# Kernel tuning notes

Measured on AMD Instinct MI355X. Metric: run time of the kernel, lower is better.

Reference implementation:

```python
import jax, jax.numpy as jnp
import numpy as np

B, S, H = 128, 256, 256  # batch, seq_len, hidden_size


def setup_inputs() -> dict:
    key = jax.random.key(0)
    ks = jax.random.split(key, 12)
    g = lambda k, shape, s=0.05: jax.random.normal(k, shape, jnp.float32) * s
    return {
        "x": jax.random.normal(ks[0], (B, S, 1024), jnp.float32),
        "stages": jax.random.normal(ks[1], (B, S, 67), jnp.float32),
        "timestamps": jax.random.uniform(ks[2], (B, S), jnp.float32),
        # stage_embedding: Linear(67,256)-ReLU-Linear(256,512)-ReLU-Linear(512,1024)-ReLU
        "se_w1": g(ks[3], (67, 256)), "se_b1": jnp.zeros((256,), jnp.float32),
        "se_w2": g(ks[4], (256, 512)), "se_b2": jnp.zeros((512,), jnp.float32),
        "se_w3": g(ks[5], (512, 1024)), "se_b3": jnp.zeros((1024,), jnp.float32),
        # TLSTM weights
        "W_all_w": g(ks[6], (H, 4 * H)), "W_all_b": jnp.zeros((4 * H,), jnp.float32),
        "U_all_w": g(ks[7], (2048, 4 * H)), "U_all_b": jnp.zeros((4 * H,), jnp.float32),
        "W_d_w": g(ks[8], (H, H)), "W_d_b": jnp.zeros((H,), jnp.float32),
        # classifier Linear(256,1)
        "cls_w": g(ks[9], (H, 1)), "cls_b": jnp.zeros((1,), jnp.float32),
    }


def reference(x, stages, timestamps, se_w1, se_b1, se_w2, se_b2, se_w3, se_b3,
              W_all_w, W_all_b, U_all_w, U_all_b, W_d_w, W_d_b, cls_w, cls_b):
    b, s, _ = x.shape
    # stage embedding MLP on flattened [b*s, 67]
    st = stages.reshape(b * s, 67)
    st = jax.nn.relu(st @ se_w1 + se_b1)
    st = jax.nn.relu(st @ se_w2 + se_b2)
    st = jax.nn.relu(st @ se_w3 + se_b3)
    xin = jnp.concatenate([x, st.reshape(b, s, 1024)], axis=2)  # [b,s,2048]
    # input projection U_all for all steps at once (same math, batched GEMM)
    u = jnp.einsum('bse,eh->bsh', xin, U_all_w) + U_all_b  # [b,s,4H]
    u_t = jnp.swapaxes(u, 0, 1)                             # [s,b,4H]
    ts_t = jnp.swapaxes(timestamps, 0, 1)[..., None]        # [s,b,1]

    def step(carry, inp):
        h, c = carry
        ut, tt = inp
        c_s1 = jnp.tanh(c @ W_d_w + W_d_b)
        c_adj = (c - c_s1) + c_s1 * tt  # time-decay adjusted cell
        outs = h @ W_all_w + W_all_b + ut
        f, i, o, c_tmp = jnp.split(jax.nn.sigmoid(outs), 4, axis=1)
        c_new = f * c_adj + i * c_tmp
        h_new = o * jnp.tanh(c_new)
        return (h_new, c_new), h_new

    h0 = jnp.zeros((b, H), x.dtype)
    c0 = jnp.zeros((b, H), x.dtype)
    _, hs = jax.lax.scan(step, (h0, c0), (u_t, ts_t))  # hs: [s,b,H]
    feat = jnp.swapaxes(hs, 0, 1).reshape(b * s, H)
    out = feat @ cls_w + cls_b
    return out, feat
```

## Files before the change

kernel.cpp:

```cpp
#include <hip/hip_runtime.h>
#include <hip/hip_bf16.h>
#include <stdint.h>

#define B_ 128
#define S_ 256
#define H_ 256

typedef __attribute__((ext_vector_type(8))) short short8;
typedef __attribute__((ext_vector_type(4))) float f32x4;

__device__ __forceinline__ short f2bf_s(float x){
    union { __hip_bfloat16 b; short s; } u; u.b = __float2bfloat16(x); return u.s;
}
__device__ __forceinline__ float bf2f_s(short s){
    union { __hip_bfloat16 b; short s2; } u; u.s2 = s; return __bfloat162float(u.b);
}
__device__ __forceinline__ void load_lds16(const void* g, void* l){
    __builtin_amdgcn_global_load_lds(
        (const __attribute__((address_space(1))) void*)g,
        (__attribute__((address_space(3))) void*)l, 16, 0, 0);
}
__device__ __forceinline__ float sigmoidf_(float x){
    return 1.0f / (1.0f + __expf(-x));
}


__global__ void k_cvt_x(const float* __restrict__ x, short* __restrict__ xin){
    int q = blockIdx.x * blockDim.x + threadIdx.x;
    if (q >= 8388608) return;
    const float4 v = ((const float4*)x)[q];
    int r = q >> 8;
    int c4 = (q & 255) << 2;
    short4 o;
    o.x = f2bf_s(v.x); o.y = f2bf_s(v.y); o.z = f2bf_s(v.z); o.w = f2bf_s(v.w);
    *(short4*)(xin + (int64_t)r * 2048 + c4) = o;
}

__global__ void k_cvt_stages(const float* __restrict__ st, short* __restrict__ sp){
    int i = blockIdx.x * blockDim.x + threadIdx.x;
    if (i >= 32768 * 96) return;
    int r = i / 96, k = i - r * 96;
    sp[i] = (k < 67) ? f2bf_s(st[(int64_t)r * 67 + k]) : (short)0;
}

__global__ void k_transpose(const float* __restrict__ w, short* __restrict__ wt,
                            int K, int N, int Kpad){
    int i = blockIdx.x * blockDim.x + threadIdx.x;
    if (i >= N * Kpad) return;
    int n = i / Kpad, k = i - n * Kpad;
    wt[i] = (k < K) ? f2bf_s(w[(int64_t)k * N + n]) : (short)0;
}

__global__ __launch_bounds__(256) void k_gemm(
    const short* __restrict__ A, int lda,
    const short* __restrict__ BT, int ldb,
    const float* __restrict__ bias,
    int K, int flags,
    float* __restrict__ Cf, short* __restrict__ Cb, int ldc)
{
    __shared__ __align__(16) short At[128 * 32];
    __shared__ __align__(16) short Bt[128 * 32];
    const int tid = threadIdx.x;
    const int lane = tid & 63, w = tid >> 6;
    const int q = lane >> 4, m = lane & 15;
    const int wr = w >> 1, wc = w & 1;
    const int bm = blockIdx.y, bn = blockIdx.x;

    const short* Ablk = A + (int64_t)bm * 128 * lda;
    const short* Bblk = BT + (int64_t)bn * 128 * ldb;

    f32x4 acc[4][4] = {};

    for (int k0 = 0; k0 < K; k0 += 32){
#pragma unroll
        for (int call = 0; call < 2; ++call){
            int chunk = (call * 4 + w) * 64 + lane;
            int row = chunk >> 2, co = (chunk & 3) * 8;
            load_lds16(Ablk + (int64_t)row * lda + k0 + co, At + (call * 4 + w) * 512);
            load_lds16(Bblk + (int64_t)row * ldb + k0 + co, Bt + (call * 4 + w) * 512);
        }
        __syncthreads();
        short8 af[4], bfr[4];
#pragma unroll
        for (int mt = 0; mt < 4; ++mt)
            af[mt] = *(const short8*)(At + (wr * 64 + mt * 16 + m) * 32 + q * 8);
#pragma unroll
        for (int nt = 0; nt < 4; ++nt)
            bfr[nt] = *(const short8*)(Bt + (wc * 64 + nt * 16 + m) * 32 + q * 8);
#pragma unroll
        for (int mt = 0; mt < 4; ++mt)
#pragma unroll
            for (int nt = 0; nt < 4; ++nt)
                acc[mt][nt] = __builtin_amdgcn_mfma_f32_16x16x32_bf16(
                    af[mt], bfr[nt], acc[mt][nt], 0, 0, 0);
        __syncthreads();
    }

#pragma unroll
    for (int mt = 0; mt < 4; ++mt){
#pragma unroll
        for (int nt = 0; nt < 4; ++nt){
            int col = bn * 128 + wc * 64 + nt * 16 + m;
            float bv = bias[col];
#pragma unroll
            for (int rg = 0; rg < 4; ++rg){
                int row = bm * 128 + wr * 64 + mt * 16 + q * 4 + rg;
                float v = acc[mt][nt][rg] + bv;
                if (flags & 1) v = fmaxf(v, 0.0f);
                if (flags & 2){
                    Cb[(int64_t)row * ldc + col] = f2bf_s(v);
                } else if (flags & 4){
                    int s = row & 255, b = row >> 8;
                    Cf[((int64_t)s * 128 + b) * 1024 + col] = v;
                } else {
                    Cf[(int64_t)row * ldc + col] = v;
                }
            }
        }
    }
}

__global__ __launch_bounds__(256, 2) void k_scan(
    const float* __restrict__ W_all, const float* __restrict__ W_all_b,
    const float* __restrict__ W_d,   const float* __restrict__ W_d_b,
    const float* __restrict__ u,     const float* __restrict__ tsp,
    unsigned* __restrict__ ctr,
    unsigned* __restrict__ h_seq,
    unsigned* __restrict__ c_seq,
    float* __restrict__ feat)
{
    __shared__ __align__(16) short wf_hi[3][8][64][8];
    __shared__ __align__(16) short wf_lo[3][8][64][8];
    __shared__ float Dg[3][16][17];

    const int tid = threadIdx.x;
    const int r = blockIdx.x >> 5, cg = blockIdx.x & 31;
    const int j0 = cg * 8, row0 = r * 16;

    for (int idx = tid; idx < 3 * 8 * 64; idx += 256){
        int t = idx / 512;
        int kk = (idx >> 6) & 7;
        int ln = idx & 63;
        int qq = ln >> 4, nn = ln & 15;
#pragma unroll
        for (int jj = 0; jj < 8; ++jj){
            int k = kk * 32 + qq * 8 + jj;
            float v = 0.0f;
            if (t < 2){
                int ngl = (nn < 8) ? (t * 512 + j0 + nn) : (t * 512 + 256 + j0 + nn - 8);
                v = W_all[(int64_t)k * 1024 + ngl];
            } else if (nn < 8){
                v = W_d[(int64_t)k * 256 + j0 + nn];
            }
            short hi = f2bf_s(v);
            wf_hi[t][kk][ln][jj] = hi;
            wf_lo[t][kk][ln][jj] = f2bf_s(v - bf2f_s(hi));
        }
    }
    __syncthreads();

    const int lane = tid & 63, w = tid >> 6;
    const int q = lane >> 4, al15 = lane & 15;

    const int b_own  = tid >> 3;
    const int jl_own = tid & 7;
    const int gb     = row0 + b_own;
    const int gj     = j0 + jl_own;
    float c_reg = 0.0f;

    float bf_ = 0, bi_ = 0, bo_ = 0, bg_ = 0, bd_ = 0;
    if (tid < 128){
        bf_ = W_all_b[gj];
        bi_ = W_all_b[256 + gj];
        bo_ = W_all_b[512 + gj];
        bg_ = W_all_b[768 + gj];
        bd_ = W_d_b[gj];
    }

    for (int s = 0; s < 256; ++s){
        float uf = 0, ui = 0, uo = 0, ug = 0, tt = 0;
        if (tid < 128){
            const float* urow = u + ((int64_t)s * 128 + gb) * 1024;
            uf = urow[gj];       ui = urow[256 + gj];
            uo = urow[512 + gj]; ug = urow[768 + gj];
            tt = tsp[gb * 256 + s];
        }

        if (s > 0 && tid == 0){
            while (__hip_atomic_fetch_add(&ctr[r * 256 + s - 1], 0u,
                                          __ATOMIC_RELAXED, __HIP_MEMORY_SCOPE_AGENT) < 32u)
                ;
        }
        __syncthreads();

        if (w < 3){
            const unsigned* src = (w < 2 ? h_seq : c_seq) + (int64_t)s * 32768
                                  + (row0 + al15) * 256;
            f32x4 acc = {0.0f, 0.0f, 0.0f, 0.0f};
#pragma unroll
            for (int kk = 0; kk < 8; ++kk){
                int kb = kk * 32 + q * 8;
                const uint4* p = (const uint4*)(src + kb);
                uint4 da = p[0], db = p[1];
                unsigned w0 = da.x, w1 = da.y, w2 = da.z, w3 = da.w;
                unsigned w4 = db.x, w5 = db.y, w6 = db.z, w7 = db.w;
                union { short8 v; unsigned u32[4]; } ah, al;
                ah.u32[0] = __builtin_amdgcn_perm(w1, w0, 0x05040100u);
                ah.u32[1] = __builtin_amdgcn_perm(w3, w2, 0x05040100u);
                ah.u32[2] = __builtin_amdgcn_perm(w5, w4, 0x05040100u);
                ah.u32[3] = __builtin_amdgcn_perm(w7, w6, 0x05040100u);
                al.u32[0] = __builtin_amdgcn_perm(w1, w0, 0x07060302u);
                al.u32[1] = __builtin_amdgcn_perm(w3, w2, 0x07060302u);
                al.u32[2] = __builtin_amdgcn_perm(w5, w4, 0x07060302u);
                al.u32[3] = __builtin_amdgcn_perm(w7, w6, 0x07060302u);
                short8 bh = *(const short8*)&wf_hi[w][kk][lane][0];
                short8 bl = *(const short8*)&wf_lo[w][kk][lane][0];
                acc = __builtin_amdgcn_mfma_f32_16x16x32_bf16(ah.v, bh, acc, 0, 0, 0);
                acc = __builtin_amdgcn_mfma_f32_16x16x32_bf16(ah.v, bl, acc, 0, 0, 0);
                acc = __builtin_amdgcn_mfma_f32_16x16x32_bf16(al.v, bh, acc, 0, 0, 0);
            }
#pragma unroll
            for (int rg = 0; rg < 4; ++rg)
                Dg[w][q * 4 + rg][al15] = acc[rg];
        }
        __syncthreads();

        if (tid < 128){
            float fpre = Dg[0][b_own][jl_own]     + uf + bf_;
            float ipre = Dg[0][b_own][8 + jl_own] + ui + bi_;
            float opre = Dg[1][b_own][jl_own]     + uo + bo_;
            float gpre = Dg[1][b_own][8 + jl_own] + ug + bg_;
            float spre = Dg[2][b_own][jl_own]     + bd_;

            float cs1 = tanhf(spre);
            float cadj = (c_reg - cs1) + cs1 * tt;
            float fg = sigmoidf_(fpre);
            float ig = sigmoidf_(ipre);
            float og = sigmoidf_(opre);
            float gg = sigmoidf_(gpre);
            float cn = fg * cadj + ig * gg;
            float hn = og * tanhf(cn);
            c_reg = cn;

            short chi = f2bf_s(cn);
            unsigned cword = (unsigned)(unsigned short)chi |
                             ((unsigned)(unsigned short)f2bf_s(cn - bf2f_s(chi)) << 16);
            short hhi = f2bf_s(hn);
            unsigned hword = (unsigned)(unsigned short)hhi |
                             ((unsigned)(unsigned short)f2bf_s(hn - bf2f_s(hhi)) << 16);
            int64_t oidx = (int64_t)(s + 1) * 32768 + gb * 256 + gj;
            __hip_atomic_store(&c_seq[oidx], cword,
                               __ATOMIC_RELAXED, __HIP_MEMORY_SCOPE_AGENT);
            __hip_atomic_store(&h_seq[oidx], hword,
                               __ATOMIC_RELAXED, __HIP_MEMORY_SCOPE_AGENT);
            __builtin_nontemporal_store(hn, &feat[((int64_t)gb * 256 + s) * 256 + gj]);
        }
        __syncthreads();
        if (tid == 0)
            __hip_atomic_fetch_add(&ctr[r * 256 + s], 1u,
                                   __ATOMIC_RELAXED, __HIP_MEMORY_SCOPE_AGENT);
    }
}

__global__ __launch_bounds__(256) void k_cls(
    const float* __restrict__ feat, const float* __restrict__ cls_w,
    const float* __restrict__ cls_b, float* __restrict__ out)
{
    int tid = threadIdx.x, lane = tid & 63, w = tid >> 6;
    int row = blockIdx.x * 4 + w;
    float4 v  = ((const float4*)(feat + (int64_t)row * 256))[lane];
    float4 cw = ((const float4*)cls_w)[lane];
    float d = v.x * cw.x + v.y * cw.y + v.z * cw.z + v.w * cw.w;
#pragma unroll
    for (int off = 32; off > 0; off >>= 1)
        d += __shfl_down(d, off, 64);
    if (lane == 0) out[row] = d + cls_b[0];
}

extern "C" void kernel_launch(void* const* d_in, const int* in_sizes, int n_in,
                              void* d_out, int out_size, void* d_ws, size_t ws_size,
                              hipStream_t stream) {
    const float* x      = (const float*)d_in[0];
    const float* stages = (const float*)d_in[1];
    const float* tsp    = (const float*)d_in[2];
    const float* se_w1  = (const float*)d_in[3];
    const float* se_b1  = (const float*)d_in[4];
    const float* se_w2  = (const float*)d_in[5];
    const float* se_b2  = (const float*)d_in[6];
    const float* se_w3  = (const float*)d_in[7];
    const float* se_b3  = (const float*)d_in[8];
    const float* W_all  = (const float*)d_in[9];
    const float* W_allb = (const float*)d_in[10];
    const float* U_w    = (const float*)d_in[11];
    const float* U_b    = (const float*)d_in[12];
    const float* W_d    = (const float*)d_in[13];
    const float* W_d_b  = (const float*)d_in[14];
    const float* cls_w  = (const float*)d_in[15];
    const float* cls_b  = (const float*)d_in[16];
    (void)in_sizes; (void)n_in; (void)out_size; (void)ws_size;

    float* out  = (float*)d_out;
    float* feat = out + 32768;

    char* ws = (char*)d_ws;
    unsigned* ctr    = (unsigned*)(ws + 0);
    short*  stagesP  = (short*)  (ws + 532480);
    short*  st1      = (short*)  (ws + 6823936);
    short*  st2      = (short*)  (ws + 23601152);
    short*  w1T      = (short*)  (ws + 57155584);
    short*  w2T      = (short*)  (ws + 57204736);
    short*  w3T      = (short*)  (ws + 57466880);
    short*  UwT      = (short*)  (ws + 58515456);
    short*  xin      = (short*)  (ws + 62709760);
    float*  u        = (float*)  (ws + 196927488);
    unsigned* h_seq  = (unsigned*)(ws + 62709760);
    unsigned* c_seq  = (unsigned*)(ws + 62709760 + 33685504);

    hipMemsetAsync(ctr, 0, 8192, stream);

    k_cvt_x<<<8388608 / 256, 256, 0, stream>>>(x, xin);
    k_cvt_stages<<<(32768 * 96) / 256, 256, 0, stream>>>(stages, stagesP);
    k_transpose<<<(256 * 96) / 256, 256, 0, stream>>>(se_w1, w1T, 67, 256, 96);
    k_transpose<<<(512 * 256) / 256, 256, 0, stream>>>(se_w2, w2T, 256, 512, 256);
    k_transpose<<<(1024 * 512) / 256, 256, 0, stream>>>(se_w3, w3T, 512, 1024, 512);
    k_transpose<<<(1024 * 2048) / 256, 256, 0, stream>>>(U_w, UwT, 2048, 1024, 2048);

    k_gemm<<<dim3(2, 256), 256, 0, stream>>>(stagesP, 96, w1T, 96, se_b1, 96, 1 | 2,
                                             nullptr, st1, 256);
    k_gemm<<<dim3(4, 256), 256, 0, stream>>>(st1, 256, w2T, 256, se_b2, 256, 1 | 2,
                                             nullptr, st2, 512);
    k_gemm<<<dim3(8, 256), 256, 0, stream>>>(st2, 512, w3T, 512, se_b3, 512, 1 | 2,
                                             nullptr, xin + 1024, 2048);
    k_gemm<<<dim3(8, 256), 256, 0, stream>>>(xin, 2048, UwT, 2048, U_b, 2048, 4,
                                             u, nullptr, 1024);

    hipMemsetAsync(h_seq, 0, 131072, stream);
    hipMemsetAsync(c_seq, 0, 131072, stream);

    k_scan<<<256, 256, 0, stream>>>(W_all, W_allb, W_d, W_d_b, u, tsp,
                                    ctr, h_seq, c_seq, feat);

    k_cls<<<8192, 256, 0, stream>>>(feat, cls_w, cls_b, out);
}
```

Measured before the change: 1.484 ms.

## Overlap U_all projection GEMM with recurrent scan via fused persistent kernel

The input projection GEMM is split. The first 32 row-blocks (time steps 0–31) run up front, and the remaining row-blocks run as extra workgroups inside a fused kernel alongside the scan blocks. Scan blocks poll per-row-block progress counters before reading u. Inputs are written in time-major order so GEMM row-blocks map to time steps. The per-step counter barrier is replaced with a double-buffered h/c ring whose low mantissa bits carry a step tag, and consumers spin on the tagged data directly. The aim is to hide most of the big GEMM behind the latency-bound scan and cut one synchronization round trip per step, at the cost of slightly perturbing the low bits of h/c and relying on all 2048 blocks being co-resident or scheduled scan-first.

After: 2.783 ms. 87.6% more time.

```diff
diff --git a/kernel.cpp b/kernel.cpp
--- a/kernel.cpp
+++ b/kernel.cpp
@@ -31,9 +31,10 @@
     const float4 v = ((const float4*)x)[q];
     int r = q >> 8;
     int c4 = (q & 255) << 2;
+    int rp = (r & 255) * 128 + (r >> 8);
     short4 o;
     o.x = f2bf_s(v.x); o.y = f2bf_s(v.y); o.z = f2bf_s(v.z); o.w = f2bf_s(v.w);
-    *(short4*)(xin + (int64_t)r * 2048 + c4) = o;
+    *(short4*)(xin + (int64_t)rp * 2048 + c4) = o;
 }
 
 __global__ void k_cvt_stages(const float* __restrict__ st, short* __restrict__ sp){
@@ -108,10 +109,9 @@
                 float v = acc[mt][nt][rg] + bv;
                 if (flags & 1) v = fmaxf(v, 0.0f);
                 if (flags & 2){
-                    Cb[(int64_t)row * ldc + col] = f2bf_s(v);
-                } else if (flags & 4){
-                    int s = row & 255, b = row >> 8;
-                    Cf[((int64_t)s * 128 + b) * 1024 + col] = v;
+                    int64_t orow = (flags & 8)
+                        ? ((int64_t)(row & 255) * 128 + (row >> 8)) : (int64_t)row;
+                    Cb[orow * ldc + col] = f2bf_s(v);
                 } else {
                     Cf[(int64_t)row * ldc + col] = v;
                 }
@@ -120,20 +120,83 @@
     }
 }
 
-__global__ __launch_bounds__(256, 2) void k_scan(
+struct ScanSh {
+    short wf_hi[3][8][64][8];
+    short wf_lo[3][8][64][8];
+    float Dg[3][16][17];
+};
+struct GemmSh { short At[128 * 32]; short Bt[128 * 32]; };
+
+__global__ __launch_bounds__(256, 2) void k_fused(
+    const short* __restrict__ xin, const short* __restrict__ UwT,
+    const float* __restrict__ U_b,
     const float* __restrict__ W_all, const float* __restrict__ W_all_b,
     const float* __restrict__ W_d,   const float* __restrict__ W_d_b,
-    const float* __restrict__ u,     const float* __restrict__ tsp,
-    unsigned* __restrict__ ctr,
-    unsigned* __restrict__ h_seq,
-    unsigned* __restrict__ c_seq,
+    float* uu,
+    const float* __restrict__ tsp,
+    unsigned* __restrict__ uprog,
+    unsigned* __restrict__ hring,
+    unsigned* __restrict__ cring,
     float* __restrict__ feat)
 {
-    __shared__ __align__(16) short wf_hi[3][8][64][8];
-    __shared__ __align__(16) short wf_lo[3][8][64][8];
-    __shared__ float Dg[3][16][17];
-
+    __shared__ __align__(16) union { ScanSh sc; GemmSh gm; } sh;
     const int tid = threadIdx.x;
+
+    if (blockIdx.x >= 256){
+        int gid = blockIdx.x - 256;
+        const int bm = 32 + (gid >> 3), bn = gid & 7;
+        const int lane = tid & 63, w = tid >> 6;
+        const int q = lane >> 4, m = lane & 15;
+        const int wr = w >> 1, wc = w & 1;
+        const short* Ablk = xin + (int64_t)bm * 128 * 2048;
+        const short* Bblk = UwT + (int64_t)bn * 128 * 2048;
+        f32x4 acc[4][4] = {};
+        for (int k0 = 0; k0 < 2048; k0 += 32){
+#pragma unroll
+            for (int call = 0; call < 2; ++call){
+                int chunk = (call * 4 + w) * 64 + lane;
+                int row = chunk >> 2, co = (chunk & 3) * 8;
+                load_lds16(Ablk + (int64_t)row * 2048 + k0 + co, sh.gm.At + (call * 4 + w) * 512);
+                load_lds16(Bblk + (int64_t)row * 2048 + k0 + co, sh.gm.Bt + (call * 4 + w) * 512);
+            }
+            __syncthreads();
+            short8 af[4], bfr[4];
+#pragma unroll
+            for (int mt = 0; mt < 4; ++mt)
+                af[mt] = *(const short8*)(sh.gm.At + (wr * 64 + mt * 16 + m) * 32 + q * 8);
+#pragma unroll
+            for (int nt = 0; nt < 4; ++nt)
+                bfr[nt] = *(const short8*)(sh.gm.Bt + (wc * 64 + nt * 16 + m) * 32 + q * 8);
+#pragma unroll
+            for (int mt = 0; mt < 4; ++mt)
+#pragma unroll
+                for (int nt = 0; nt < 4; ++nt)
+                    acc[mt][nt] = __builtin_amdgcn_mfma_f32_16x16x32_bf16(
+                        af[mt], bfr[nt], acc[mt][nt], 0, 0, 0);
+            __syncthreads();
+        }
+#pragma unroll
+        for (int mt = 0; mt < 4; ++mt)
+#pragma unroll
+            for (int nt = 0; nt < 4; ++nt){
+                int col = bn * 128 + wc * 64 + nt * 16 + m;
+                float bv = U_b[col];
+#pragma unroll
+                for (int rg = 0; rg < 4; ++rg){
+                    int row = bm * 128 + wr * 64 + mt * 16 + q * 4 + rg;
+                    __hip_atomic_store(&uu[(int64_t)row * 1024 + col],
+                                       acc[mt][nt][rg] + bv,
+                                       __ATOMIC_RELAXED, __HIP_MEMORY_SCOPE_AGENT);
+                }
+            }
+        __syncthreads();
+        if (tid == 0)
+            __hip_atomic_fetch_add(&uprog[bm], 1u,
+                                   __ATOMIC_RELAXED, __HIP_MEMORY_SCOPE_AGENT);
+        return;
+    }
+
+    __builtin_amdgcn_s_setprio(1);
     const int r = blockIdx.x >> 5, cg = blockIdx.x & 31;
     const int j0 = cg * 8, row0 = r * 16;
 
@@ -153,8 +216,8 @@
                 v = W_d[(int64_t)k * 256 + j0 + nn];
             }
             short hi = f2bf_s(v);
-            wf_hi[t][kk][ln][jj] = hi;
-            wf_lo[t][kk][ln][jj] = f2bf_s(v - bf2f_s(hi));
+            sh.sc.wf_hi[t][kk][ln][jj] = hi;
+            sh.sc.wf_lo[t][kk][ln][jj] = f2bf_s(v - bf2f_s(hi));
         }
     }
     __syncthreads();
@@ -162,75 +225,152 @@
     const int lane = tid & 63, w = tid >> 6;
     const int q = lane >> 4, al15 = lane & 15;
 
-    const int b_own  = tid >> 3;
-    const int jl_own = tid & 7;
-    const int gb     = row0 + b_own;
-    const int gj     = j0 + jl_own;
+    const int tid2 = tid & 127;
+    const int b_own = tid2 >> 3, jl_own = tid2 & 7;
+    const int gb = row0 + b_own, gj = j0 + jl_own;
     float c_reg = 0.0f;
-
     float bf_ = 0, bi_ = 0, bo_ = 0, bg_ = 0, bd_ = 0;
-    if (tid < 128){
+    if (w >= 2){
         bf_ = W_all_b[gj];
         bi_ = W_all_b[256 + gj];
         bo_ = W_all_b[512 + gj];
         bg_ = W_all_b[768 + gj];
         bd_ = W_d_b[gj];
     }
+    int u_upto = 32;
+
+    const unsigned long long TAGM = 0xFFFCFFFFFFFCFFFFULL;
 
     for (int s = 0; s < 256; ++s){
+        __syncthreads();
         float uf = 0, ui = 0, uo = 0, ug = 0, tt = 0;
-        if (tid < 128){
-            const float* urow = u + ((int64_t)s * 128 + gb) * 1024;
+
+        if (w < 2){
+            f32x4 acc0 = {0.f, 0.f, 0.f, 0.f}, acc1 = {0.f, 0.f, 0.f, 0.f};
+            if (s > 0){
+                const unsigned tagexp = (unsigned)((s - 1) & 3);
+                unsigned long long* sp = (unsigned long long*)
+                    ((w == 0 ? hring : cring) + (((s - 1) & 1) << 15) + (row0 + al15) * 256);
+                unsigned long long d[32];
+                for (unsigned round = 0; ; ++round){
+                    if ((round & 3u) != 3u){
+#pragma unroll
+                        for (int kk = 0; kk < 8; ++kk)
+#pragma unroll
+                            for (int i = 0; i < 4; ++i)
+                                d[kk * 4 + i] = __hip_atomic_load(
+                                    &sp[kk * 16 + q * 4 + i],
+                                    __ATOMIC_RELAXED, __HIP_MEMORY_SCOPE_AGENT);
+                    } else {
+#pragma unroll
+                        for (int kk = 0; kk < 8; ++kk)
+#pragma unroll
+                            for (int i = 0; i < 4; ++i){
+                                unsigned* pw = (unsigned*)&sp[kk * 16 + q * 4 + i];
+                                unsigned lo = __hip_atomic_fetch_add(pw, 0u,
+                                    __ATOMIC_RELAXED, __HIP_MEMORY_SCOPE_AGENT);
+                                unsigned hi = __hip_atomic_fetch_add(pw + 1, 0u,
+                                    __ATOMIC_RELAXED, __HIP_MEMORY_SCOPE_AGENT);
+                                d[kk * 4 + i] = (unsigned long long)lo |
+                                                ((unsigned long long)hi << 32);
+                            }
+                    }
+                    bool bad = false;
+#pragma unroll
+                    for (int t2 = 0; t2 < 32; ++t2){
+                        unsigned lo = (unsigned)d[t2], hi = (unsigned)(d[t2] >> 32);
+                        bad |= (((lo >> 16) & 3u) != tagexp) | (((hi >> 16) & 3u) != tagexp);
+                    }
+                    if (__all(!bad)) break;
+                }
+                if (w == 0){
+#pragma unroll
+                    for (int kk = 0; kk < 8; ++kk){
+                        unsigned long long q0 = d[kk*4+0] & TAGM, q1 = d[kk*4+1] & TAGM;
+                        unsigned long long q2 = d[kk*4+2] & TAGM, q3 = d[kk*4+3] & TAGM;
+                        unsigned w0_=(unsigned)q0, w1_=(unsigned)(q0>>32);
+                        unsigned w2_=(unsigned)q1, w3_=(unsigned)(q1>>32);
+                        unsigned w4_=(unsigned)q2, w5_=(unsigned)(q2>>32);
+                        unsigned w6_=(unsigned)q3, w7_=(unsigned)(q3>>32);
+                        union { short8 v; unsigned u32[4]; } ah, al;
+                        ah.u32[0]=__builtin_amdgcn_perm(w1_,w0_,0x05040100u);
+                        ah.u32[1]=__builtin_amdgcn_perm(w3_,w2_,0x05040100u);
+                        ah.u32[2]=__builtin_amdgcn_perm(w5_,w4_,0x05040100u);
+                        ah.u32[3]=__builtin_amdgcn_perm(w7_,w6_,0x05040100u);
+                        al.u32[0]=__builtin_amdgcn_perm(w1_,w0_,0x07060302u);
+                        al.u32[1]=__builtin_amdgcn_perm(w3_,w2_,0x07060302u);
+                        al.u32[2]=__builtin_amdgcn_perm(w5_,w4_,0x07060302u);
+                        al.u32[3]=__builtin_amdgcn_perm(w7_,w6_,0x07060302u);
+                        short8 bh0 = *(const short8*)&sh.sc.wf_hi[0][kk][lane][0];
+                        short8 bl0 = *(const short8*)&sh.sc.wf_lo[0][kk][lane][0];
+                        short8 bh1 = *(const short8*)&sh.sc.wf_hi[1][kk][lane][0];
+                        short8 bl1 = *(const short8*)&sh.sc.wf_lo[1][kk][lane][0];
+                        acc0 = __builtin_amdgcn_mfma_f32_16x16x32_bf16(ah.v, bh0, acc0, 0,0,0);
+                        acc0 = __builtin_amdgcn_mfma_f32_16x16x32_bf16(ah.v, bl0, acc0, 0,0,0);
+                        acc0 = __builtin_amdgcn_mfma_f32_16x16x32_bf16(al.v, bh0, acc0, 0,0,0);
+                        acc1 = __builtin_amdgcn_mfma_f32_16x16x32_bf16(ah.v, bh1, acc1, 0,0,0);
+                        acc1 = __builtin_amdgcn_mfma_f32_16x16x32_bf16(ah.v, bl1, acc1, 0,0,0);
+                        acc1 = __builtin_amdgcn_mfma_f32_16x16x32_bf16(al.v, bh1, acc1, 0,0,0);
+                    }
+                } else {
+#pragma unroll
+                    for (int kk = 0; kk < 8; ++kk){
+                        unsigned long long q0 = d[kk*4+0] & TAGM, q1 = d[kk*4+1] & TAGM;
+                        unsigned long long q2 = d[kk*4+2] & TAGM, q3 = d[kk*4+3] & TAGM;
+                        unsigned w0_=(unsigned)q0, w1_=(unsigned)(q0>>32);
+                        unsigned w2_=(unsigned)q1, w3_=(unsigned)(q1>>32);
+                        unsigned w4_=(unsigned)q2, w5_=(unsigned)(q2>>32);
+                        unsigned w6_=(unsigned)q3, w7_=(unsigned)(q3>>32);
+                        union { short8 v; unsigned u32[4]; } ah, al;
+                        ah.u32[0]=__builtin_amdgcn_perm(w1_,w0_,0x05040100u);
+                        ah.u32[1]=__builtin_amdgcn_perm(w3_,w2_,0x05040100u);
+                        ah.u32[2]=__builtin_amdgcn_perm(w5_,w4_,0x05040100u);
+                        ah.u32[3]=__builtin_amdgcn_perm(w7_,w6_,0x05040100u);
+                        al.u32[0]=__builtin_amdgcn_perm(w1_,w0_,0x07060302u);
+                        al.u32[1]=__builtin_amdgcn_perm(w3_,w2_,0x07060302u);
+                        al.u32[2]=__builtin_amdgcn_perm(w5_,w4_,0x07060302u);
+                        al.u32[3]=__builtin_amdgcn_perm(w7_,w6_,0x07060302u);
+                        short8 bh2 = *(const short8*)&sh.sc.wf_hi[2][kk][lane][0];
+                        short8 bl2 = *(const short8*)&sh.sc.wf_lo[2][kk][lane][0];
+                        acc0 = __builtin_amdgcn_mfma_f32_16x16x32_bf16(ah.v, bh2, acc0, 0,0,0);
+                        acc0 = __builtin_amdgcn_mfma_f32_16x16x32_bf16(ah.v, bl2, acc0, 0,0,0);
+                        acc0 = __builtin_amdgcn_mfma_f32_16x16x32_bf16(al.v, bh2, acc0, 0,0,0);
+                    }
+                }
+            }
+#pragma unroll
+            for (int rg = 0; rg < 4; ++rg){
+                if (w == 0){
+                    sh.sc.Dg[0][q * 4 + rg][al15] = acc0[rg];
+                    sh.sc.Dg[1][q * 4 + rg][al15] = acc1[rg];
+                } else {
+                    sh.sc.Dg[2][q * 4 + rg][al15] = acc0[rg];
+                }
+            }
+        } else {
+            bool adv = false; unsigned rr = 0;
+            while (u_upto <= s){
+                unsigned v = ((rr & 3u) != 3u)
+                    ? __hip_atomic_load(&uprog[u_upto],
+                                        __ATOMIC_RELAXED, __HIP_MEMORY_SCOPE_AGENT)
+                    : __hip_atomic_fetch_add(&uprog[u_upto], 0u,
+                                        __ATOMIC_RELAXED, __HIP_MEMORY_SCOPE_AGENT);
+                if (v >= 8u){ ++u_upto; adv = true; } else ++rr;
+            }
+            if (adv) __builtin_amdgcn_fence(__ATOMIC_ACQUIRE, "agent");
+            const float* urow = uu + ((int64_t)s * 128 + gb) * 1024;
             uf = urow[gj];       ui = urow[256 + gj];
             uo = urow[512 + gj]; ug = urow[768 + gj];
             tt = tsp[gb * 256 + s];
         }
-
-        if (s > 0 && tid == 0){
-            while (__hip_atomic_fetch_add(&ctr[r * 256 + s - 1], 0u,
-                                          __ATOMIC_RELAXED, __HIP_MEMORY_SCOPE_AGENT) < 32u)
-                ;
-        }
         __syncthreads();
 
-        if (w < 3){
-            const unsigned* src = (w < 2 ? h_seq : c_seq) + (int64_t)s * 32768
-                                  + (row0 + al15) * 256;
-            f32x4 acc = {0.0f, 0.0f, 0.0f, 0.0f};
-#pragma unroll
-            for (int kk = 0; kk < 8; ++kk){
-                int kb = kk * 32 + q * 8;
-                const uint4* p = (const uint4*)(src + kb);
-                uint4 da = p[0], db = p[1];
-                unsigned w0 = da.x, w1 = da.y, w2 = da.z, w3 = da.w;
-                unsigned w4 = db.x, w5 = db.y, w6 = db.z, w7 = db.w;
-                union { short8 v; unsigned u32[4]; } ah, al;
-                ah.u32[0] = __builtin_amdgcn_perm(w1, w0, 0x05040100u);
-                ah.u32[1] = __builtin_amdgcn_perm(w3, w2, 0x05040100u);
-                ah.u32[2] = __builtin_amdgcn_perm(w5, w4, 0x05040100u);
-                ah.u32[3] = __builtin_amdgcn_perm(w7, w6, 0x05040100u);
-                al.u32[0] = __builtin_amdgcn_perm(w1, w0, 0x07060302u);
-                al.u32[1] = __builtin_amdgcn_perm(w3, w2, 0x07060302u);
-                al.u32[2] = __builtin_amdgcn_perm(w5, w4, 0x07060302u);
-                al.u32[3] = __builtin_amdgcn_perm(w7, w6, 0x07060302u);
-                short8 bh = *(const short8*)&wf_hi[w][kk][lane][0];
-                short8 bl = *(const short8*)&wf_lo[w][kk][lane][0];
-                acc = __builtin_amdgcn_mfma_f32_16x16x32_bf16(ah.v, bh, acc, 0, 0, 0);
-                acc = __builtin_amdgcn_mfma_f32_16x16x32_bf16(ah.v, bl, acc, 0, 0, 0);
-                acc = __builtin_amdgcn_mfma_f32_16x16x32_bf16(al.v, bh, acc, 0, 0, 0);
-            }
-#pragma unroll
-            for (int rg = 0; rg < 4; ++rg)
-                Dg[w][q * 4 + rg][al15] = acc[rg];
-        }
-        __syncthreads();
-
-        if (tid < 128){
-            float fpre = Dg[0][b_own][jl_own]     + uf + bf_;
-            float ipre = Dg[0][b_own][8 + jl_own] + ui + bi_;
-            float opre = Dg[1][b_own][jl_own]     + uo + bo_;
-            float gpre = Dg[1][b_own][8 + jl_own] + ug + bg_;
-            float spre = Dg[2][b_own][jl_own]     + bd_;
+        if (w >= 2){
+            float fpre = sh.sc.Dg[0][b_own][jl_own]     + uf + bf_;
+            float ipre = sh.sc.Dg[0][b_own][8 + jl_own] + ui + bi_;
+            float opre = sh.sc.Dg[1][b_own][jl_own]     + uo + bo_;
+            float gpre = sh.sc.Dg[1][b_own][8 + jl_own] + ug + bg_;
+            float spre = sh.sc.Dg[2][b_own][jl_own]     + bd_;
 
             float cs1 = tanhf(spre);
             float cadj = (c_reg - cs1) + cs1 * tt;
@@ -242,23 +382,22 @@
             float hn = og * tanhf(cn);
             c_reg = cn;
 
+            unsigned tag = (unsigned)(s & 3);
             short chi = f2bf_s(cn);
+            unsigned short clo = (unsigned short)f2bf_s(cn - bf2f_s(chi));
             unsigned cword = (unsigned)(unsigned short)chi |
-                             ((unsigned)(unsigned short)f2bf_s(cn - bf2f_s(chi)) << 16);
+                             (((unsigned)((clo & 0xFFFCu) | tag)) << 16);
             short hhi = f2bf_s(hn);
+            unsigned short hlo = (unsigned short)f2bf_s(hn - bf2f_s(hhi));
             unsigned hword = (unsigned)(unsigned short)hhi |
-                             ((unsigned)(unsigned short)f2bf_s(hn - bf2f_s(hhi)) << 16);
-            int64_t oidx = (int64_t)(s + 1) * 32768 + gb * 256 + gj;
-            __hip_atomic_store(&c_seq[oidx], cword,
+                             (((unsigned)((hlo & 0xFFFCu) | tag)) << 16);
+            int off = ((s & 1) << 15) + gb * 256 + gj;
+            __hip_atomic_store(&cring[off], cword,
                                __ATOMIC_RELAXED, __HIP_MEMORY_SCOPE_AGENT);
-            __hip_atomic_store(&h_seq[oidx], hword,
+            __hip_atomic_store(&hring[off], hword,
                                __ATOMIC_RELAXED, __HIP_MEMORY_SCOPE_AGENT);
             __builtin_nontemporal_store(hn, &feat[((int64_t)gb * 256 + s) * 256 + gj]);
         }
-        __syncthreads();
-        if (tid == 0)
-            __hip_atomic_fetch_add(&ctr[r * 256 + s], 1u,
-                                   __ATOMIC_RELAXED, __HIP_MEMORY_SCOPE_AGENT);
     }
 }
 
@@ -303,7 +442,9 @@
     float* feat = out + 32768;
 
     char* ws = (char*)d_ws;
-    unsigned* ctr    = (unsigned*)(ws + 0);
+    unsigned* uprog  = (unsigned*)(ws + 0);
+    unsigned* hring  = (unsigned*)(ws + 4096);
+    unsigned* cring  = (unsigned*)(ws + 266240);
     short*  stagesP  = (short*)  (ws + 532480);
     short*  st1      = (short*)  (ws + 6823936);
     short*  st2      = (short*)  (ws + 23601152);
@@ -313,10 +454,12 @@
     short*  UwT      = (short*)  (ws + 58515456);
     short*  xin      = (short*)  (ws + 62709760);
     float*  u        = (float*)  (ws + 196927488);
-    unsigned* h_seq  = (unsigned*)(ws + 62709760);
-    unsigned* c_seq  = (unsigned*)(ws + 62709760 + 33685504);
-
-    hipMemsetAsync(ctr, 0, 8192, stream);
+
+    hipMemsetAsync(uprog, 0, 4096, stream);
+    hipMemsetAsync((char*)hring,          0x55, 131072, stream);
+    hipMemsetAsync((char*)hring + 131072, 0x00, 131072, stream);
+    hipMemsetAsync((char*)cring,          0x55, 131072, stream);
+    hipMemsetAsync((char*)cring + 131072, 0x00, 131072, stream);
 
     k_cvt_x<<<8388608 / 256, 256, 0, stream>>>(x, xin);
     k_cvt_stages<<<(32768 * 96) / 256, 256, 0, stream>>>(stages, stagesP);
@@ -329,16 +472,14 @@
                                              nullptr, st1, 256);
     k_gemm<<<dim3(4, 256), 256, 0, stream>>>(st1, 256, w2T, 256, se_b2, 256, 1 | 2,
                                              nullptr, st2, 512);
-    k_gemm<<<dim3(8, 256), 256, 0, stream>>>(st2, 512, w3T, 512, se_b3, 512, 1 | 2,
+    k_gemm<<<dim3(8, 256), 256, 0, stream>>>(st2, 512, w3T, 512, se_b3, 512, 1 | 2 | 8,
                                              nullptr, xin + 1024, 2048);
-    k_gemm<<<dim3(8, 256), 256, 0, stream>>>(xin, 2048, UwT, 2048, U_b, 2048, 4,
-                                             u, nullptr, 1024);
-
-    hipMemsetAsync(h_seq, 0, 131072, stream);
-    hipMemsetAsync(c_seq, 0, 131072, stream);
-
-    k_scan<<<256, 256, 0, stream>>>(W_all, W_allb, W_d, W_d_b, u, tsp,
-                                    ctr, h_seq, c_seq, feat);
+
+    k_gemm<<<dim3(8, 32), 256, 0, stream>>>(xin, 2048, UwT, 2048, U_b, 2048, 0,
+                                            u, nullptr, 1024);
+
+    k_fused<<<2048, 256, 0, stream>>>(xin, UwT, U_b, W_all, W_allb, W_d, W_d_b,
+                                      u, tsp, uprog, hring, cring, feat);
 
     k_cls<<<8192, 256, 0, stream>>>(feat, cls_w, cls_b, out);
 }
```

## Permute xin rows to step-major early and rebalance scan warp roles

Applied to the files above, without the earlier changes.

The x conversion and the third stage-MLP GEMM now write xin rows in (s,b) order, so the U projection GEMM stores u with contiguous row-major writes instead of a scattered transposed store. In the scan kernel, the gate matmuls move from three warps to two (warp 0 handles both W_all tiles) and the elementwise cell update moves to warps 2-3. The spin-wait gets an iteration cap, an explicit acquire fence is added, and launch bounds drop to one block per SIMD pair. The iteration cap risks proceeding before data is ready if a wait runs long, and warp 0 now carries a heavier serial MFMA chain per step.

Result: slower. 2.551 ms (+71.9%).

```diff
diff --git a/kernel.cpp b/kernel.cpp
--- a/kernel.cpp
+++ b/kernel.cpp
@@ -31,9 +31,10 @@
     const float4 v = ((const float4*)x)[q];
     int r = q >> 8;
     int c4 = (q & 255) << 2;
+    int rp = (r & 255) * 128 + (r >> 8);
     short4 o;
     o.x = f2bf_s(v.x); o.y = f2bf_s(v.y); o.z = f2bf_s(v.z); o.w = f2bf_s(v.w);
-    *(short4*)(xin + (int64_t)r * 2048 + c4) = o;
+    *(short4*)(xin + (int64_t)rp * 2048 + c4) = o;
 }
 
 __global__ void k_cvt_stages(const float* __restrict__ st, short* __restrict__ sp){
@@ -108,10 +109,9 @@
                 float v = acc[mt][nt][rg] + bv;
                 if (flags & 1) v = fmaxf(v, 0.0f);
                 if (flags & 2){
-                    Cb[(int64_t)row * ldc + col] = f2bf_s(v);
-                } else if (flags & 4){
-                    int s = row & 255, b = row >> 8;
-                    Cf[((int64_t)s * 128 + b) * 1024 + col] = v;
+                    int64_t orow = (flags & 8)
+                        ? ((int64_t)(row & 255) * 128 + (row >> 8)) : (int64_t)row;
+                    Cb[orow * ldc + col] = f2bf_s(v);
                 } else {
                     Cf[(int64_t)row * ldc + col] = v;
                 }
@@ -120,7 +120,7 @@
     }
 }
 
-__global__ __launch_bounds__(256, 2) void k_scan(
+__global__ __launch_bounds__(256, 1) void k_scan(
     const float* __restrict__ W_all, const float* __restrict__ W_all_b,
     const float* __restrict__ W_d,   const float* __restrict__ W_d_b,
     const float* __restrict__ u,     const float* __restrict__ tsp,
@@ -162,14 +162,12 @@
     const int lane = tid & 63, w = tid >> 6;
     const int q = lane >> 4, al15 = lane & 15;
 
-    const int b_own  = tid >> 3;
-    const int jl_own = tid & 7;
-    const int gb     = row0 + b_own;
-    const int gj     = j0 + jl_own;
+    const int tid2 = tid & 127;
+    const int b_own = tid2 >> 3, jl_own = tid2 & 7;
+    const int gb = row0 + b_own, gj = j0 + jl_own;
     float c_reg = 0.0f;
-
     float bf_ = 0, bi_ = 0, bo_ = 0, bg_ = 0, bd_ = 0;
-    if (tid < 128){
+    if (w >= 2){
         bf_ = W_all_b[gj];
         bi_ = W_all_b[256 + gj];
         bo_ = W_all_b[512 + gj];
@@ -179,53 +177,78 @@
 
     for (int s = 0; s < 256; ++s){
         float uf = 0, ui = 0, uo = 0, ug = 0, tt = 0;
-        if (tid < 128){
+
+        if (w >= 2){
             const float* urow = u + ((int64_t)s * 128 + gb) * 1024;
             uf = urow[gj];       ui = urow[256 + gj];
             uo = urow[512 + gj]; ug = urow[768 + gj];
             tt = tsp[gb * 256 + s];
         }
-
         if (s > 0 && tid == 0){
-            while (__hip_atomic_fetch_add(&ctr[r * 256 + s - 1], 0u,
-                                          __ATOMIC_RELAXED, __HIP_MEMORY_SCOPE_AGENT) < 32u)
-                ;
-        }
-        __syncthreads();
-
-        if (w < 3){
-            const unsigned* src = (w < 2 ? h_seq : c_seq) + (int64_t)s * 32768
-                                  + (row0 + al15) * 256;
-            f32x4 acc = {0.0f, 0.0f, 0.0f, 0.0f};
+            for (unsigned it = 0; it < 100000u; ++it){
+                if (__hip_atomic_fetch_add(&ctr[r * 256 + s - 1], 0u,
+                                           __ATOMIC_RELAXED,
+                                           __HIP_MEMORY_SCOPE_AGENT) >= 32u)
+                    break;
+            }
+        }
+        __syncthreads();
+
+        if (w < 2){
+            if (s > 0)
+                __builtin_amdgcn_fence(__ATOMIC_ACQUIRE, "agent");
+
+            const unsigned* src = (w == 0 ? h_seq : c_seq)
+                                  + (int64_t)s * 32768 + (row0 + al15) * 256;
+            f32x4 acc0 = {0.f, 0.f, 0.f, 0.f}, acc1 = {0.f, 0.f, 0.f, 0.f};
 #pragma unroll
             for (int kk = 0; kk < 8; ++kk){
                 int kb = kk * 32 + q * 8;
                 const uint4* p = (const uint4*)(src + kb);
                 uint4 da = p[0], db = p[1];
-                unsigned w0 = da.x, w1 = da.y, w2 = da.z, w3 = da.w;
-                unsigned w4 = db.x, w5 = db.y, w6 = db.z, w7 = db.w;
+                unsigned w0_ = da.x, w1_ = da.y, w2_ = da.z, w3_ = da.w;
+                unsigned w4_ = db.x, w5_ = db.y, w6_ = db.z, w7_ = db.w;
                 union { short8 v; unsigned u32[4]; } ah, al;
-                ah.u32[0] = __builtin_amdgcn_perm(w1, w0, 0x05040100u);
-                ah.u32[1] = __builtin_amdgcn_perm(w3, w2, 0x05040100u);
-                ah.u32[2] = __builtin_amdgcn_perm(w5, w4, 0x05040100u);
-                ah.u32[3] = __builtin_amdgcn_perm(w7, w6, 0x05040100u);
-                al.u32[0] = __builtin_amdgcn_perm(w1, w0, 0x07060302u);
-                al.u32[1] = __builtin_amdgcn_perm(w3, w2, 0x07060302u);
-                al.u32[2] = __builtin_amdgcn_perm(w5, w4, 0x07060302u);
-                al.u32[3] = __builtin_amdgcn_perm(w7, w6, 0x07060302u);
-                short8 bh = *(const short8*)&wf_hi[w][kk][lane][0];
-                short8 bl = *(const short8*)&wf_lo[w][kk][lane][0];
-                acc = __builtin_amdgcn_mfma_f32_16x16x32_bf16(ah.v, bh, acc, 0, 0, 0);
-                acc = __builtin_amdgcn_mfma_f32_16x16x32_bf16(ah.v, bl, acc, 0, 0, 0);
-                acc = __builtin_amdgcn_mfma_f32_16x16x32_bf16(al.v, bh, acc, 0, 0, 0);
-            }
-#pragma unroll
-            for (int rg = 0; rg < 4; ++rg)
-                Dg[w][q * 4 + rg][al15] = acc[rg];
-        }
-        __syncthreads();
-
-        if (tid < 128){
+                ah.u32[0] = __builtin_amdgcn_perm(w1_, w0_, 0x05040100u);
+                ah.u32[1] = __builtin_amdgcn_perm(w3_, w2_, 0x05040100u);
+                ah.u32[2] = __builtin_amdgcn_perm(w5_, w4_, 0x05040100u);
+                ah.u32[3] = __builtin_amdgcn_perm(w7_, w6_, 0x05040100u);
+                al.u32[0] = __builtin_amdgcn_perm(w1_, w0_, 0x07060302u);
+                al.u32[1] = __builtin_amdgcn_perm(w3_, w2_, 0x07060302u);
+                al.u32[2] = __builtin_amdgcn_perm(w5_, w4_, 0x07060302u);
+                al.u32[3] = __builtin_amdgcn_perm(w7_, w6_, 0x07060302u);
+                if (w == 0){
+                    short8 bh0 = *(const short8*)&wf_hi[0][kk][lane][0];
+                    short8 bl0 = *(const short8*)&wf_lo[0][kk][lane][0];
+                    short8 bh1 = *(const short8*)&wf_hi[1][kk][lane][0];
+                    short8 bl1 = *(const short8*)&wf_lo[1][kk][lane][0];
+                    acc0 = __builtin_amdgcn_mfma_f32_16x16x32_bf16(ah.v, bh0, acc0, 0,0,0);
+                    acc0 = __builtin_amdgcn_mfma_f32_16x16x32_bf16(ah.v, bl0, acc0, 0,0,0);
+                    acc0 = __builtin_amdgcn_mfma_f32_16x16x32_bf16(al.v, bh0, acc0, 0,0,0);
+                    acc1 = __builtin_amdgcn_mfma_f32_16x16x32_bf16(ah.v, bh1, acc1, 0,0,0);
+                    acc1 = __builtin_amdgcn_mfma_f32_16x16x32_bf16(ah.v, bl1, acc1, 0,0,0);
+                    acc1 = __builtin_amdgcn_mfma_f32_16x16x32_bf16(al.v, bh1, acc1, 0,0,0);
+                } else {
+                    short8 bh2 = *(const short8*)&wf_hi[2][kk][lane][0];
+                    short8 bl2 = *(const short8*)&wf_lo[2][kk][lane][0];
+                    acc0 = __builtin_amdgcn_mfma_f32_16x16x32_bf16(ah.v, bh2, acc0, 0,0,0);
+                    acc0 = __builtin_amdgcn_mfma_f32_16x16x32_bf16(ah.v, bl2, acc0, 0,0,0);
+                    acc0 = __builtin_amdgcn_mfma_f32_16x16x32_bf16(al.v, bh2, acc0, 0,0,0);
+                }
+            }
+#pragma unroll
+            for (int rg = 0; rg < 4; ++rg){
+                if (w == 0){
+                    Dg[0][q * 4 + rg][al15] = acc0[rg];
+                    Dg[1][q * 4 + rg][al15] = acc1[rg];
+                } else {
+                    Dg[2][q * 4 + rg][al15] = acc0[rg];
+                }
+            }
+        }
+        __syncthreads();
+
+        if (w >= 2){
             float fpre = Dg[0][b_own][jl_own]     + uf + bf_;
             float ipre = Dg[0][b_own][8 + jl_own] + ui + bi_;
             float opre = Dg[1][b_own][jl_own]     + uo + bo_;
@@ -256,7 +279,8 @@
             __builtin_nontemporal_store(hn, &feat[((int64_t)gb * 256 + s) * 256 + gj]);
         }
         __syncthreads();
-        if (tid == 0)
+
+        if (tid == 128)
             __hip_atomic_fetch_add(&ctr[r * 256 + s], 1u,
                                    __ATOMIC_RELAXED, __HIP_MEMORY_SCOPE_AGENT);
     }
@@ -329,9 +353,10 @@
                                              nullptr, st1, 256);
     k_gemm<<<dim3(4, 256), 256, 0, stream>>>(st1, 256, w2T, 256, se_b2, 256, 1 | 2,
                                              nullptr, st2, 512);
-    k_gemm<<<dim3(8, 256), 256, 0, stream>>>(st2, 512, w3T, 512, se_b3, 512, 1 | 2,
+    k_gemm<<<dim3(8, 256), 256, 0, stream>>>(st2, 512, w3T, 512, se_b3, 512, 1 | 2 | 8,
                                              nullptr, xin + 1024, 2048);
-    k_gemm<<<dim3(8, 256), 256, 0, stream>>>(xin, 2048, UwT, 2048, U_b, 2048, 4,
+
+    k_gemm<<<dim3(8, 256), 256, 0, stream>>>(xin, 2048, UwT, 2048, U_b, 2048, 0,
                                              u, nullptr, 1024);
 
     hipMemsetAsync(h_seq, 0, 131072, stream);
```
